# Kernel optimization log

Hardware: AMD Instinct MI355X
Metric: run time of the kernel (lower is better)

Reference implementation:

```python
import jax, jax.numpy as jnp
import numpy as np


def _construct_adj(adj, weight_cross_time):
    # adj: (N, N); weight_cross_time: (S-1, N, N) -> local_adj: (S*N, S*N)
    N = adj.shape[0]
    S = weight_cross_time.shape[0] + 1
    local_adj = jnp.zeros((S * N, S * N), dtype=adj.dtype)
    for i in range(S):  # diagonal blocks (small fixed loop over strides)
        local_adj = local_adj.at[i * N:(i + 1) * N, i * N:(i + 1) * N].set(adj)
    for k in range(S - 1):  # cross-time blocks, symmetric placement
        wk = weight_cross_time[k]
        local_adj = local_adj.at[k * N:(k + 1) * N, (k + 1) * N:(k + 2) * N].set(wk)
        local_adj = local_adj.at[(k + 1) * N:(k + 2) * N, k * N:(k + 1) * N].set(wk.T)
    return local_adj


def setup_inputs() -> dict:
    key = jax.random.key(0)
    k1, k2, k3, k4 = jax.random.split(key, 4)
    N, S, B, Cin, Cout = 1024, 3, 32, 64, 64
    # xavier_uniform-like scales for the learned adjacency parameters
    s_adj = float(np.sqrt(6.0 / (N + N)))
    x = jax.random.normal(k1, (S * N, B, Cin), dtype=jnp.float32)
    adj = jax.random.uniform(k2, (N, N), dtype=jnp.float32, minval=-s_adj, maxval=s_adj)
    weight_cross_time = jax.random.uniform(k3, (S - 1, N, N), dtype=jnp.float32, minval=-s_adj, maxval=s_adj)
    s_fc = float(np.sqrt(1.0 / Cin))
    W = jax.random.uniform(k4, (Cin, 2 * Cout), dtype=jnp.float32, minval=-s_fc, maxval=s_fc)
    b = jnp.zeros((2 * Cout,), dtype=jnp.float32)
    return {"x": x, "adj": adj, "weight_cross_time": weight_cross_time, "W": W, "b": b}


def reference(x, adj, weight_cross_time, W, b):
    # Faithful translation of gcn_operation.forward with activation='GLU'.
    Cout = W.shape[-1] // 2
    local_adj = _construct_adj(adj, weight_cross_time)          # (S*N, S*N)
    h = jnp.einsum('nm,mbc->nbc', local_adj, x)                  # (S*N, B, Cin)
    lhs_rhs = h @ W + b                                          # (S*N, B, 2*Cout)
    lhs, rhs = lhs_rhs[..., :Cout], lhs_rhs[..., Cout:]
    return lhs * jax.nn.sigmoid(rhs)                             # (S*N, B, Cout)
```

## Files before the change

kernel.cpp:

```cpp
#include <hip/hip_runtime.h>

typedef unsigned short u16;
typedef unsigned int   u32;
typedef __attribute__((ext_vector_type(8))) short short8;
typedef __attribute__((ext_vector_type(4))) float f32x4;

__device__ __forceinline__ u16 f2bf(float f) {
    u32 u = __float_as_uint(f);
    u = (u + 0x7fffu + ((u >> 16) & 1u)) >> 16;
    return (u16)u;
}

__device__ __forceinline__ void gld_lds16(const void* g, void* l) {
    __builtin_amdgcn_global_load_lds(
        (const __attribute__((address_space(1))) u32*)g,
        (__attribute__((address_space(3))) u32*)l, 16, 0, 0);
}

__global__ __launch_bounds__(256) void prep_kernel(
    const float* __restrict__ x, const float* __restrict__ adj,
    const float* __restrict__ wct, const float* __restrict__ W,
    u16* __restrict__ Ab, u16* __restrict__ W0T, u16* __restrict__ W1T,
    u16* __restrict__ Xt, u16* __restrict__ Wt)
{
    __shared__ float tile[64][65];
    const int t = threadIdx.x;
    const int bid = blockIdx.x;

    if (bid < 3072) {
        const int i4 = bid * 256 + t;
        const float4 v = (i4 < 262144) ? ((const float4*)adj)[i4]
                                       : ((const float4*)wct)[i4 - 262144];
        ushort4 o;
        o.x = f2bf(v.x); o.y = f2bf(v.y); o.z = f2bf(v.z); o.w = f2bf(v.w);
        ((ushort4*)Ab)[i4] = o;
        return;
    }

    const float* src; u16* dst; int C, R, r0, c0;
    if (bid < 3328)      { const int q = bid - 3072; src = wct;           dst = W0T; C = 1024; R = 1024; r0 = (q & 15) << 6; c0 = (q >> 4) << 6; }
    else if (bid < 3584) { const int q = bid - 3328; src = wct + 1048576; dst = W1T; C = 1024; R = 1024; r0 = (q & 15) << 6; c0 = (q >> 4) << 6; }
    else if (bid < 5120) { const int q = bid - 3584; src = x;             dst = Xt;  C = 2048; R = 3072; r0 = (q % 48) << 6; c0 = (q / 48) << 6; }
    else                 { const int q = bid - 5120; src = W;             dst = Wt;  C = 128;  R = 64;   r0 = 0;             c0 = q << 6; }

#pragma unroll
    for (int it = 0; it < 4; ++it) {
        const int f4 = it * 256 + t;
        const int r  = f4 >> 4;
        const int c4 = (f4 & 15) << 2;
        const float4 v = *(const float4*)&src[(size_t)(r0 + r) * C + c0 + c4];
        tile[r][c4]     = v.x; tile[r][c4 + 1] = v.y;
        tile[r][c4 + 2] = v.z; tile[r][c4 + 3] = v.w;
    }
    __syncthreads();
#pragma unroll
    for (int it = 0; it < 4; ++it) {
        const int f4 = it * 256 + t;
        const int u  = f4 >> 4;
        const int v4 = (f4 & 15) << 2;
        ushort4 o;
        o.x = f2bf(tile[v4][u]);     o.y = f2bf(tile[v4 + 1][u]);
        o.z = f2bf(tile[v4 + 2][u]); o.w = f2bf(tile[v4 + 3][u]);
        *(ushort4*)&dst[(size_t)(c0 + u) * R + r0 + v4] = o;
    }
}

__global__ __launch_bounds__(256, 3) void gemm_h_kernel(
    const u16* __restrict__ Ab,  const u16* __restrict__ W0b,
    const u16* __restrict__ W1b, const u16* __restrict__ W0T,
    const u16* __restrict__ W1T, const u16* __restrict__ Xt,
    const u16* __restrict__ Wt,  const float* __restrict__ bias,
    float* __restrict__ out)
{
    __shared__ u16 Asm[64 * 64];
    __shared__ u16 Bsm[128 * 64];
    __shared__ u16 Wsm[128 * 64];
    __shared__ float Bias_sm[128];

    const int tid = threadIdx.x;
    const int bid = blockIdx.x;
    const int xcd = bid & 7;
    const int idx = bid >> 3;
    const int i   = idx >> 5;
    const int idp = idx & 31;
    const int row0 = (idp & 15) << 6;
    const int nt   = xcd * 2 + (idp >> 4);
    const int col0 = nt << 7;

    const int l    = tid & 63;
    const int w    = tid >> 6;
    const int wr   = ((tid >> 7) & 1) << 5;
    const int wc   = ((tid >> 6) & 1) << 6;
    const int lrow = l & 15;
    const int g16  = l >> 4;
    const int rsw  = lrow & 7;

    {
        u16* wdst = Wsm + ((tid & ~63) << 3);
#pragma unroll
        for (int p = 0; p < 4; ++p) {
            const int flat = p * 256 + tid;
            const int row = flat >> 3, slot = flat & 7;
            gld_lds16(Wt + row * 64 + ((slot ^ (row & 7)) << 3), wdst + p * 2048);
        }
        if (tid < 128) Bias_sm[tid] = bias[tid];
    }

    const int sub  = tid >> 3;
    const int srck = ((tid & 7) ^ (sub & 7)) << 3;
    u16* AsmW = Asm + ((tid >> 6) << 9);
    u16* BsmW = Bsm + ((tid >> 6) << 9);

    f32x4 acc[2][4] = {};

    auto run_term = [&](const u16* __restrict__ Amat, const u16* __restrict__ Bmat) {
        for (int k0 = 0; k0 < 1024; k0 += 64) {
            const u16* ga = Amat + (size_t)sub * 1024 + k0 + srck;
            gld_lds16(ga,             AsmW);
            gld_lds16(ga + 32 * 1024, AsmW + 2048);
            const u16* gb = Bmat + (size_t)sub * 3072 + k0 + srck;
            gld_lds16(gb,             BsmW);
            gld_lds16(gb + 32 * 3072, BsmW + 2048);
            gld_lds16(gb + 64 * 3072, BsmW + 4096);
            gld_lds16(gb + 96 * 3072, BsmW + 6144);
            __syncthreads();

            short8 af[2][2], bfr[2][4];
#pragma unroll
            for (int kk = 0; kk < 2; ++kk) {
                const int so = (((kk << 2) | g16) ^ rsw) << 3;
#pragma unroll
                for (int fm = 0; fm < 2; ++fm)
                    af[kk][fm] = *(const short8*)&Asm[(wr + fm * 16 + lrow) * 64 + so];
#pragma unroll
                for (int fn = 0; fn < 4; ++fn)
                    bfr[kk][fn] = *(const short8*)&Bsm[(wc + fn * 16 + lrow) * 64 + so];
            }
#pragma unroll
            for (int kk = 0; kk < 2; ++kk)
#pragma unroll
                for (int fm = 0; fm < 2; ++fm)
#pragma unroll
                    for (int fn = 0; fn < 4; ++fn)
                        acc[fm][fn] = __builtin_amdgcn_mfma_f32_16x16x32_bf16(
                            af[kk][fm], bfr[kk][fn], acc[fm][fn], 0, 0, 0);
            __syncthreads();
        }
    };

    const size_t xbase = (size_t)col0 * 3072;
    if (i == 0) {
        run_term(Ab  + row0 * 1024, Xt + xbase);
        run_term(W0b + row0 * 1024, Xt + xbase + 1024);
    } else if (i == 1) {
        run_term(W0T + row0 * 1024, Xt + xbase);
        run_term(Ab  + row0 * 1024, Xt + xbase + 1024);
        run_term(W1b + row0 * 1024, Xt + xbase + 2048);
    } else {
        run_term(W1T + row0 * 1024, Xt + xbase + 1024);
        run_term(Ab  + row0 * 1024, Xt + xbase + 2048);
    }

    u16* Hsm = Bsm;
#pragma unroll
    for (int fm = 0; fm < 2; ++fm)
#pragma unroll
        for (int fn = 0; fn < 4; ++fn)
#pragma unroll
            for (int r = 0; r < 4; ++r) {
                const int n   = wr + fm * 16 + (g16 << 2) + r;
                const int col = wc + fn * 16 + lrow;
                const int sl2 = ((col >> 3) ^ (n & 7));
                Hsm[n * 128 + (sl2 << 3) + (col & 7)] = f2bf(acc[fm][fn][r]);
            }
    __syncthreads();

    f32x4 acc2[2][8];
#pragma unroll
    for (int fm2 = 0; fm2 < 2; ++fm2)
#pragma unroll
        for (int fn = 0; fn < 8; ++fn) {
            const float bv = Bias_sm[fn * 16 + lrow];
            acc2[fm2][fn] = (f32x4){bv, bv, bv, bv};
        }
#pragma unroll
    for (int kk = 0; kk < 2; ++kk) {
        const int gg = (kk << 2) | g16;
        short8 ah[2], bw[8];
#pragma unroll
        for (int fm2 = 0; fm2 < 2; ++fm2) {
            const int rowp = (w << 5) + (fm2 << 4) + lrow;
            const int b = rowp >> 6, n = rowp & 63;
            const int sl2 = ((b << 3) | gg) ^ (n & 7);
            ah[fm2] = *(const short8*)&Hsm[n * 128 + (sl2 << 3)];
        }
#pragma unroll
        for (int fn = 0; fn < 8; ++fn) {
            const int c = (fn << 4) + lrow;
            const int sl2 = gg ^ (c & 7);
            bw[fn] = *(const short8*)&Wsm[c * 64 + (sl2 << 3)];
        }
#pragma unroll
        for (int fm2 = 0; fm2 < 2; ++fm2)
#pragma unroll
            for (int fn = 0; fn < 8; ++fn)
                acc2[fm2][fn] = __builtin_amdgcn_mfma_f32_16x16x32_bf16(
                    ah[fm2], bw[fn], acc2[fm2][fn], 0, 0, 0);
    }

    const int n0g = i * 1024 + row0;
    const int b0  = nt << 1;
#pragma unroll
    for (int fm2 = 0; fm2 < 2; ++fm2)
#pragma unroll
        for (int fn = 0; fn < 4; ++fn)
#pragma unroll
            for (int r = 0; r < 4; ++r) {
                const int rowp = (w << 5) + (fm2 << 4) + (g16 << 2) + r;
                const int b = rowp >> 6, nl = rowp & 63;
                const float lhs = acc2[fm2][fn][r];
                const float rhs = acc2[fm2][fn + 4][r];
                const float sg  = 1.0f / (1.0f + __expf(-rhs));
                const int c = (fn << 4) + lrow;
                out[((size_t)(n0g + nl) * 32 + (b0 + b)) * 64 + c] = lhs * sg;
            }
}

extern "C" void kernel_launch(void* const* d_in, const int* in_sizes, int n_in,
                              void* d_out, int out_size, void* d_ws, size_t ws_size,
                              hipStream_t stream)
{
    const float* x    = (const float*)d_in[0];
    const float* adj  = (const float*)d_in[1];
    const float* wct  = (const float*)d_in[2];
    const float* W    = (const float*)d_in[3];
    const float* bias = (const float*)d_in[4];
    float* out = (float*)d_out;

    char* ws = (char*)d_ws;
    u16* Xt  = (u16*)ws;
    u16* Ab  = (u16*)(ws + 12582912);
    u16* W0b = Ab + 1048576;
    u16* W1b = Ab + 2097152;
    u16* W0T = (u16*)(ws + 18874368);
    u16* W1T = W0T + 1048576;
    u16* Wt  = (u16*)(ws + 23068672);

    prep_kernel<<<5122, 256, 0, stream>>>(x, adj, wct, W, Ab, W0T, W1T, Xt, Wt);
    gemm_h_kernel<<<768, 256, 0, stream>>>(Ab, W0b, W1b, W0T, W1T, Xt, Wt, bias, out);
}
```

Baseline: 59.91 us.

## Double-buffer LDS tiles in GEMM main loop and defer W staging to epilogue

The GEMM k-loop now uses ping-pong LDS buffers for the A and B tiles. The next tile's global-to-LDS loads are issued before the MFMAs on the current tile, which drops one barrier per iteration and lets memory latency overlap compute, including across term boundaries. The W tile is no longer kept in its own LDS array for the whole kernel; it is loaded into the freed A buffer after the main loop. Total LDS per block grows (48KB+ vs 40KB), which may limit occupancy at 3 blocks/CU, and the W load now sits on the critical path before the second GEMM.

Measured after the change: 57.63 us. 1.04x faster.

```diff
diff --git a/kernel.cpp b/kernel.cpp
--- a/kernel.cpp
+++ b/kernel.cpp
@@ -72,9 +72,8 @@
     const u16* __restrict__ Wt,  const float* __restrict__ bias,
     float* __restrict__ out)
 {
-    __shared__ u16 Asm[64 * 64];
-    __shared__ u16 Bsm[128 * 64];
-    __shared__ u16 Wsm[128 * 64];
+    __shared__ u16 Adb[8192];
+    __shared__ u16 Bdb[16384];
     __shared__ float Bias_sm[128];
 
     const int tid = threadIdx.x;
@@ -95,73 +94,87 @@
     const int g16  = l >> 4;
     const int rsw  = lrow & 7;
 
-    {
-        u16* wdst = Wsm + ((tid & ~63) << 3);
-#pragma unroll
-        for (int p = 0; p < 4; ++p) {
-            const int flat = p * 256 + tid;
-            const int row = flat >> 3, slot = flat & 7;
-            gld_lds16(Wt + row * 64 + ((slot ^ (row & 7)) << 3), wdst + p * 2048);
-        }
-        if (tid < 128) Bias_sm[tid] = bias[tid];
-    }
-
     const int sub  = tid >> 3;
     const int srck = ((tid & 7) ^ (sub & 7)) << 3;
-    u16* AsmW = Asm + ((tid >> 6) << 9);
-    u16* BsmW = Bsm + ((tid >> 6) << 9);
-
+    const int wofs = w << 9;
+
+    if (tid < 128) Bias_sm[tid] = bias[tid];
+
+    u16 *Ac = Adb, *Ap = Adb + 4096, *Bc = Bdb, *Bp = Bdb + 8192;
     f32x4 acc[2][4] = {};
 
-    auto run_term = [&](const u16* __restrict__ Amat, const u16* __restrict__ Bmat) {
-        for (int k0 = 0; k0 < 1024; k0 += 64) {
-            const u16* ga = Amat + (size_t)sub * 1024 + k0 + srck;
-            gld_lds16(ga,             AsmW);
-            gld_lds16(ga + 32 * 1024, AsmW + 2048);
-            const u16* gb = Bmat + (size_t)sub * 3072 + k0 + srck;
-            gld_lds16(gb,             BsmW);
-            gld_lds16(gb + 32 * 3072, BsmW + 2048);
-            gld_lds16(gb + 64 * 3072, BsmW + 4096);
-            gld_lds16(gb + 96 * 3072, BsmW + 6144);
-            __syncthreads();
-
-            short8 af[2][2], bfr[2][4];
-#pragma unroll
-            for (int kk = 0; kk < 2; ++kk) {
-                const int so = (((kk << 2) | g16) ^ rsw) << 3;
-#pragma unroll
-                for (int fm = 0; fm < 2; ++fm)
-                    af[kk][fm] = *(const short8*)&Asm[(wr + fm * 16 + lrow) * 64 + so];
+    auto stageA = [&](u16* dst, const u16* ta, int kel) {
+        const u16* ga = ta + (size_t)sub * 1024 + kel + srck;
+        gld_lds16(ga,             dst + wofs);
+        gld_lds16(ga + 32 * 1024, dst + wofs + 2048);
+    };
+    auto stageB = [&](u16* dst, const u16* tb, int kel) {
+        const u16* gb = tb + (size_t)sub * 3072 + kel + srck;
+        gld_lds16(gb,             dst + wofs);
+        gld_lds16(gb + 32 * 3072, dst + wofs + 2048);
+        gld_lds16(gb + 64 * 3072, dst + wofs + 4096);
+        gld_lds16(gb + 96 * 3072, dst + wofs + 6144);
+    };
+    auto step = [&](const u16* pfa, const u16* pfb, int kel, int do_pf) {
+        if (do_pf) { stageA(Ap, pfa, kel); stageB(Bp, pfb, kel); }
+        short8 af[2][2], bfr[2][4];
+#pragma unroll
+        for (int kk = 0; kk < 2; ++kk) {
+            const int so = (((kk << 2) | g16) ^ rsw) << 3;
+#pragma unroll
+            for (int fm = 0; fm < 2; ++fm)
+                af[kk][fm] = *(const short8*)&Ac[(wr + fm * 16 + lrow) * 64 + so];
+#pragma unroll
+            for (int fn = 0; fn < 4; ++fn)
+                bfr[kk][fn] = *(const short8*)&Bc[(wc + fn * 16 + lrow) * 64 + so];
+        }
+#pragma unroll
+        for (int kk = 0; kk < 2; ++kk)
+#pragma unroll
+            for (int fm = 0; fm < 2; ++fm)
 #pragma unroll
                 for (int fn = 0; fn < 4; ++fn)
-                    bfr[kk][fn] = *(const short8*)&Bsm[(wc + fn * 16 + lrow) * 64 + so];
-            }
-#pragma unroll
-            for (int kk = 0; kk < 2; ++kk)
-#pragma unroll
-                for (int fm = 0; fm < 2; ++fm)
-#pragma unroll
-                    for (int fn = 0; fn < 4; ++fn)
-                        acc[fm][fn] = __builtin_amdgcn_mfma_f32_16x16x32_bf16(
-                            af[kk][fm], bfr[kk][fn], acc[fm][fn], 0, 0, 0);
-            __syncthreads();
-        }
+                    acc[fm][fn] = __builtin_amdgcn_mfma_f32_16x16x32_bf16(
+                        af[kk][fm], bfr[kk][fn], acc[fm][fn], 0, 0, 0);
+        __syncthreads();
+        u16* t;
+        t = Ac; Ac = Ap; Ap = t;
+        t = Bc; Bc = Bp; Bp = t;
+    };
+    auto run16 = [&](const u16* ta, const u16* tb,
+                     const u16* na, const u16* nb, int hn) {
+        for (int k = 1; k < 16; ++k) step(ta, tb, k << 6, 1);
+        step(na, nb, 0, hn);
     };
 
     const size_t xbase = (size_t)col0 * 3072;
+    const u16 *a0, *b0, *a1, *b1, *a2 = 0, *b2 = 0;
+    int three = 0;
     if (i == 0) {
-        run_term(Ab  + row0 * 1024, Xt + xbase);
-        run_term(W0b + row0 * 1024, Xt + xbase + 1024);
+        a0 = Ab  + row0 * 1024; b0 = Xt + xbase;
+        a1 = W0b + row0 * 1024; b1 = Xt + xbase + 1024;
     } else if (i == 1) {
-        run_term(W0T + row0 * 1024, Xt + xbase);
-        run_term(Ab  + row0 * 1024, Xt + xbase + 1024);
-        run_term(W1b + row0 * 1024, Xt + xbase + 2048);
+        a0 = W0T + row0 * 1024; b0 = Xt + xbase;
+        a1 = Ab  + row0 * 1024; b1 = Xt + xbase + 1024;
+        a2 = W1b + row0 * 1024; b2 = Xt + xbase + 2048;
+        three = 1;
     } else {
-        run_term(W1T + row0 * 1024, Xt + xbase + 1024);
-        run_term(Ab  + row0 * 1024, Xt + xbase + 2048);
-    }
-
-    u16* Hsm = Bsm;
+        a0 = W1T + row0 * 1024; b0 = Xt + xbase + 1024;
+        a1 = Ab  + row0 * 1024; b1 = Xt + xbase + 2048;
+    }
+
+    stageA(Ac, a0, 0); stageB(Bc, b0, 0);
+    __syncthreads();
+    run16(a0, b0, a1, b1, 1);
+    if (three) { run16(a1, b1, a2, b2, 1); run16(a2, b2, 0, 0, 0); }
+    else       { run16(a1, b1, 0, 0, 0); }
+
+    u16* Wsm = Adb;
+    u16* Hsm = Bdb;
+#pragma unroll
+    for (int p = 0; p < 4; ++p)
+        gld_lds16(Wt + (size_t)(p * 32 + sub) * 64 + srck,
+                  Adb + p * 2048 + wofs);
 #pragma unroll
     for (int fm = 0; fm < 2; ++fm)
 #pragma unroll
@@ -209,7 +222,7 @@
     }
 
     const int n0g = i * 1024 + row0;
-    const int b0  = nt << 1;
+    const int b0i = nt << 1;
 #pragma unroll
     for (int fm2 = 0; fm2 < 2; ++fm2)
 #pragma unroll
@@ -222,7 +235,7 @@
                 const float rhs = acc2[fm2][fn + 4][r];
                 const float sg  = 1.0f / (1.0f + __expf(-rhs));
                 const int c = (fn << 4) + lrow;
-                out[((size_t)(n0g + nl) * 32 + (b0 + b)) * 64 + c] = lhs * sg;
+                out[((size_t)(n0g + nl) * 32 + (b0i + b)) * 64 + c] = lhs * sg;
             }
 }
 
```

## Retile adjacency into MFMA fragment order, load A to registers, double-buffer B

Applied to the files above, without the earlier changes.

Prep now writes the adjacency and the transposed cross-time weights in a fragment-tiled layout, so the GEMM kernel can load A operands straight into registers with coalesced 16-byte loads and skip LDS for them. The GEMM tile changes from 64 rows by 128 columns to 128 rows by one batch (64 columns). B tiles are double-buffered in LDS, with a software prefetch that crosses term boundaries and explicit vmcnt waits in place of the full syncthreads pair. This aims to overlap global loads with MFMA and cut LDS traffic. The costs are more register pressure from holding the prefetched A fragments and hand-tuned waitcnt logic that could be fragile.

New measurement: 63.27 us. 5.6% more time.

```diff
diff --git a/kernel.cpp b/kernel.cpp
--- a/kernel.cpp
+++ b/kernel.cpp
@@ -15,6 +15,10 @@
     __builtin_amdgcn_global_load_lds(
         (const __attribute__((address_space(1))) u32*)g,
         (__attribute__((address_space(3))) u32*)l, 16, 0, 0);
+}
+
+__device__ __forceinline__ int ridx(int r, int k) {
+    return ((((r >> 4) << 7) + (k >> 3)) << 7) + ((r & 15) << 3) + (k & 7);
 }
 
 __global__ __launch_bounds__(256) void prep_kernel(
@@ -33,15 +37,19 @@
                                        : ((const float4*)wct)[i4 - 262144];
         ushort4 o;
         o.x = f2bf(v.x); o.y = f2bf(v.y); o.z = f2bf(v.z); o.w = f2bf(v.w);
-        ((ushort4*)Ab)[i4] = o;
+        const int m  = i4 >> 18;
+        const int lf = i4 & 262143;
+        const int r  = lf >> 8;
+        const int k  = (lf & 255) << 2;
+        *(ushort4*)&Ab[m * 1048576 + ridx(r, k)] = o;
         return;
     }
 
-    const float* src; u16* dst; int C, R, r0, c0;
-    if (bid < 3328)      { const int q = bid - 3072; src = wct;           dst = W0T; C = 1024; R = 1024; r0 = (q & 15) << 6; c0 = (q >> 4) << 6; }
-    else if (bid < 3584) { const int q = bid - 3328; src = wct + 1048576; dst = W1T; C = 1024; R = 1024; r0 = (q & 15) << 6; c0 = (q >> 4) << 6; }
-    else if (bid < 5120) { const int q = bid - 3584; src = x;             dst = Xt;  C = 2048; R = 3072; r0 = (q % 48) << 6; c0 = (q / 48) << 6; }
-    else                 { const int q = bid - 5120; src = W;             dst = Wt;  C = 128;  R = 64;   r0 = 0;             c0 = q << 6; }
+    const float* src; u16* dst; int C, R, r0, c0, retile;
+    if (bid < 3328)      { const int q = bid - 3072; src = wct;           dst = W0T; C = 1024; R = 1024; r0 = (q & 15) << 6; c0 = (q >> 4) << 6; retile = 1; }
+    else if (bid < 3584) { const int q = bid - 3328; src = wct + 1048576; dst = W1T; C = 1024; R = 1024; r0 = (q & 15) << 6; c0 = (q >> 4) << 6; retile = 1; }
+    else if (bid < 5120) { const int q = bid - 3584; src = x;             dst = Xt;  C = 2048; R = 3072; r0 = (q % 48) << 6; c0 = (q / 48) << 6; retile = 0; }
+    else                 { const int q = bid - 5120; src = W;             dst = Wt;  C = 128;  R = 64;   r0 = 0;             c0 = q << 6;        retile = 0; }
 
 #pragma unroll
     for (int it = 0; it < 4; ++it) {
@@ -61,7 +69,8 @@
         ushort4 o;
         o.x = f2bf(tile[v4][u]);     o.y = f2bf(tile[v4 + 1][u]);
         o.z = f2bf(tile[v4 + 2][u]); o.w = f2bf(tile[v4 + 3][u]);
-        *(ushort4*)&dst[(size_t)(c0 + u) * R + r0 + v4] = o;
+        if (retile) *(ushort4*)&dst[ridx(c0 + u, r0 + v4)] = o;
+        else        *(ushort4*)&dst[(size_t)(c0 + u) * R + r0 + v4] = o;
     }
 }
 
@@ -72,9 +81,8 @@
     const u16* __restrict__ Wt,  const float* __restrict__ bias,
     float* __restrict__ out)
 {
-    __shared__ u16 Asm[64 * 64];
-    __shared__ u16 Bsm[128 * 64];
-    __shared__ u16 Wsm[128 * 64];
+    __shared__ u16 Bdb[8192];
+    __shared__ u16 Wsm[8192];
     __shared__ float Bias_sm[128];
 
     const int tid = threadIdx.x;
@@ -83,20 +91,16 @@
     const int idx = bid >> 3;
     const int i   = idx >> 5;
     const int idp = idx & 31;
-    const int row0 = (idp & 15) << 6;
-    const int nt   = xcd * 2 + (idp >> 4);
-    const int col0 = nt << 7;
+    const int nt   = (xcd << 2) + (idp & 3);
+    const int row0 = (idp >> 2) << 7;
 
     const int l    = tid & 63;
     const int w    = tid >> 6;
-    const int wr   = ((tid >> 7) & 1) << 5;
-    const int wc   = ((tid >> 6) & 1) << 6;
     const int lrow = l & 15;
     const int g16  = l >> 4;
-    const int rsw  = lrow & 7;
 
     {
-        u16* wdst = Wsm + ((tid & ~63) << 3);
+        u16* wdst = Wsm + (w << 9);
 #pragma unroll
         for (int p = 0; p < 4; ++p) {
             const int flat = p * 256 + tid;
@@ -106,35 +110,76 @@
         if (tid < 128) Bias_sm[tid] = bias[tid];
     }
 
-    const int sub  = tid >> 3;
-    const int srck = ((tid & 7) ^ (sub & 7)) << 3;
-    u16* AsmW = Asm + ((tid >> 6) << 9);
-    u16* BsmW = Bsm + ((tid >> 6) << 9);
+    const int brow = tid >> 3;
+    const int srck = ((tid & 7) ^ (brow & 7)) << 3;
+    auto stageB = [&](u16* buf, const u16* tb, int k0) {
+        const u16* g0 = tb + (size_t)brow * 3072 + k0 + srck;
+        gld_lds16(g0,             buf + (w << 9));
+        gld_lds16(g0 + 32 * 3072, buf + (w << 9) + 2048);
+    };
+
+    const int rbw = w << 1;
+    auto loadA4 = [&](short8* d, const u16* ta, int k0) {
+        const u16* base = ta + (((rbw << 7) + (k0 >> 3)) << 7) + (l << 3);
+        d[0] = *(const short8*)(base);
+        d[1] = *(const short8*)(base + 512);
+        d[2] = *(const short8*)(base + 16384);
+        d[3] = *(const short8*)(base + 16384 + 512);
+    };
 
     f32x4 acc[2][4] = {};
-
-    auto run_term = [&](const u16* __restrict__ Amat, const u16* __restrict__ Bmat) {
-        for (int k0 = 0; k0 < 1024; k0 += 64) {
-            const u16* ga = Amat + (size_t)sub * 1024 + k0 + srck;
-            gld_lds16(ga,             AsmW);
-            gld_lds16(ga + 32 * 1024, AsmW + 2048);
-            const u16* gb = Bmat + (size_t)sub * 3072 + k0 + srck;
-            gld_lds16(gb,             BsmW);
-            gld_lds16(gb + 32 * 3072, BsmW + 2048);
-            gld_lds16(gb + 64 * 3072, BsmW + 4096);
-            gld_lds16(gb + 96 * 3072, BsmW + 6144);
-            __syncthreads();
-
-            short8 af[2][2], bfr[2][4];
+    short8 aC[4], aN[4];
+
+    const size_t xbase = (size_t)nt * 64 * 3072;
+    const u16 *ca, *cb, *na, *nb, *fa = nullptr, *fb = nullptr;
+    int nterms;
+    if (i == 0) {
+        ca = Ab  + (row0 << 10); cb = Xt + xbase;
+        na = W0b + (row0 << 10); nb = Xt + xbase + 1024;
+        nterms = 2;
+    } else if (i == 1) {
+        ca = W0T + (row0 << 10); cb = Xt + xbase;
+        na = Ab  + (row0 << 10); nb = Xt + xbase + 1024;
+        fa = W1b + (row0 << 10); fb = Xt + xbase + 2048;
+        nterms = 3;
+    } else {
+        ca = W1T + (row0 << 10); cb = Xt + xbase + 1024;
+        na = Ab  + (row0 << 10); nb = Xt + xbase + 2048;
+        nterms = 2;
+    }
+
+    stageB(Bdb, cb, 0);
+    loadA4(aC, ca, 0);
+
+    for (int t = 0; t < nterms; ++t) {
+#pragma unroll
+        for (int k = 0; k < 16; ++k) {
+            u16* bufc = Bdb + ((k & 1) << 12);
+            u16* bufp = Bdb + (((k + 1) & 1) << 12);
+            const u16* pa = (k < 15) ? ca : na;
+            const u16* pb = (k < 15) ? cb : nb;
+            const int pk0 = (k < 15) ? ((k + 1) << 6) : 0;
+            const bool pf = (k < 15) || (na != nullptr);
+
+            __builtin_amdgcn_s_barrier();
+            if (pf) {
+                stageB(bufp, pb, pk0);
+                loadA4(aN, pa, pk0);
+                asm volatile("s_waitcnt vmcnt(10)" ::: "memory");
+            } else {
+                asm volatile("s_waitcnt vmcnt(4)" ::: "memory");
+            }
+            __builtin_amdgcn_s_barrier();
+
+            short8 bfr[2][4];
 #pragma unroll
             for (int kk = 0; kk < 2; ++kk) {
-                const int so = (((kk << 2) | g16) ^ rsw) << 3;
-#pragma unroll
-                for (int fm = 0; fm < 2; ++fm)
-                    af[kk][fm] = *(const short8*)&Asm[(wr + fm * 16 + lrow) * 64 + so];
-#pragma unroll
-                for (int fn = 0; fn < 4; ++fn)
-                    bfr[kk][fn] = *(const short8*)&Bsm[(wc + fn * 16 + lrow) * 64 + so];
+                const int kidx = (kk << 2) | g16;
+#pragma unroll
+                for (int fn = 0; fn < 4; ++fn) {
+                    const int col = (fn << 4) + lrow;
+                    bfr[kk][fn] = *(const short8*)&bufc[(col << 6) + ((kidx ^ (col & 7)) << 3)];
+                }
             }
 #pragma unroll
             for (int kk = 0; kk < 2; ++kk)
@@ -143,44 +188,32 @@
 #pragma unroll
                     for (int fn = 0; fn < 4; ++fn)
                         acc[fm][fn] = __builtin_amdgcn_mfma_f32_16x16x32_bf16(
-                            af[kk][fm], bfr[kk][fn], acc[fm][fn], 0, 0, 0);
-            __syncthreads();
-        }
-    };
-
-    const size_t xbase = (size_t)col0 * 3072;
-    if (i == 0) {
-        run_term(Ab  + row0 * 1024, Xt + xbase);
-        run_term(W0b + row0 * 1024, Xt + xbase + 1024);
-    } else if (i == 1) {
-        run_term(W0T + row0 * 1024, Xt + xbase);
-        run_term(Ab  + row0 * 1024, Xt + xbase + 1024);
-        run_term(W1b + row0 * 1024, Xt + xbase + 2048);
-    } else {
-        run_term(W1T + row0 * 1024, Xt + xbase + 1024);
-        run_term(Ab  + row0 * 1024, Xt + xbase + 2048);
-    }
-
-    u16* Hsm = Bsm;
+                            aC[(fm << 1) | kk], bfr[kk][fn], acc[fm][fn], 0, 0, 0);
+#pragma unroll
+            for (int j = 0; j < 4; ++j) aC[j] = aN[j];
+        }
+        ca = na; cb = nb; na = fa; nb = fb; fa = nullptr; fb = nullptr;
+    }
+
+    __syncthreads();
+    u16* Hsm = Bdb;
 #pragma unroll
     for (int fm = 0; fm < 2; ++fm)
 #pragma unroll
         for (int fn = 0; fn < 4; ++fn)
 #pragma unroll
             for (int r = 0; r < 4; ++r) {
-                const int n   = wr + fm * 16 + (g16 << 2) + r;
-                const int col = wc + fn * 16 + lrow;
-                const int sl2 = ((col >> 3) ^ (n & 7));
-                Hsm[n * 128 + (sl2 << 3) + (col & 7)] = f2bf(acc[fm][fn][r]);
-            }
-    __syncthreads();
+                const int n   = (w << 5) + (fm << 4) + (g16 << 2) + r;
+                const int cin = (fn << 4) + lrow;
+                Hsm[(n << 6) + (((cin >> 3) ^ (n & 7)) << 3) + (cin & 7)] = f2bf(acc[fm][fn][r]);
+            }
 
     f32x4 acc2[2][8];
 #pragma unroll
     for (int fm2 = 0; fm2 < 2; ++fm2)
 #pragma unroll
         for (int fn = 0; fn < 8; ++fn) {
-            const float bv = Bias_sm[fn * 16 + lrow];
+            const float bv = Bias_sm[(fn << 4) + lrow];
             acc2[fm2][fn] = (f32x4){bv, bv, bv, bv};
         }
 #pragma unroll
@@ -189,16 +222,13 @@
         short8 ah[2], bw[8];
 #pragma unroll
         for (int fm2 = 0; fm2 < 2; ++fm2) {
-            const int rowp = (w << 5) + (fm2 << 4) + lrow;
-            const int b = rowp >> 6, n = rowp & 63;
-            const int sl2 = ((b << 3) | gg) ^ (n & 7);
-            ah[fm2] = *(const short8*)&Hsm[n * 128 + (sl2 << 3)];
+            const int n = (w << 5) + (fm2 << 4) + lrow;
+            ah[fm2] = *(const short8*)&Hsm[(n << 6) + ((gg ^ (n & 7)) << 3)];
         }
 #pragma unroll
         for (int fn = 0; fn < 8; ++fn) {
             const int c = (fn << 4) + lrow;
-            const int sl2 = gg ^ (c & 7);
-            bw[fn] = *(const short8*)&Wsm[c * 64 + (sl2 << 3)];
+            bw[fn] = *(const short8*)&Wsm[(c << 6) + ((gg ^ (c & 7)) << 3)];
         }
 #pragma unroll
         for (int fm2 = 0; fm2 < 2; ++fm2)
@@ -208,21 +238,19 @@
                     ah[fm2], bw[fn], acc2[fm2][fn], 0, 0, 0);
     }
 
-    const int n0g = i * 1024 + row0;
-    const int b0  = nt << 1;
+    const int n0g = (i << 10) + row0;
 #pragma unroll
     for (int fm2 = 0; fm2 < 2; ++fm2)
 #pragma unroll
         for (int fn = 0; fn < 4; ++fn)
 #pragma unroll
             for (int r = 0; r < 4; ++r) {
-                const int rowp = (w << 5) + (fm2 << 4) + (g16 << 2) + r;
-                const int b = rowp >> 6, nl = rowp & 63;
+                const int nl = (w << 5) + (fm2 << 4) + (g16 << 2) + r;
                 const float lhs = acc2[fm2][fn][r];
                 const float rhs = acc2[fm2][fn + 4][r];
                 const float sg  = 1.0f / (1.0f + __expf(-rhs));
                 const int c = (fn << 4) + lrow;
-                out[((size_t)(n0g + nl) * 32 + (b0 + b)) * 64 + c] = lhs * sg;
+                out[((size_t)(n0g + nl) * 32 + nt) * 64 + c] = lhs * sg;
             }
 }
 
```

## Double-buffer GEMM with 128x128 tiles and 32x32x16 MFMA

Applied to the files above, without the earlier changes.

Rewrites the main GEMM kernel to use 128x128 output tiles, shared-memory double buffering with async global-to-LDS prefetch and explicit vmcnt waits, and 32x32x16 bf16 MFMA instead of 16x16x32. The grid drops from 768 to 384 blocks, and the 3-term row segment is scheduled first. The aim is to hide load latency, raise arithmetic intensity and cut barrier overhead. The cost is higher LDS and register use, which lowers occupancy to 2 blocks per CU, and fewer blocks than the roughly 256 CUs may leave the second wave partially idle.

After: 70.92 us. 18.4% more time.

```diff
diff --git a/kernel.cpp b/kernel.cpp
--- a/kernel.cpp
+++ b/kernel.cpp
@@ -3,7 +3,7 @@
 typedef unsigned short u16;
 typedef unsigned int   u32;
 typedef __attribute__((ext_vector_type(8))) short short8;
-typedef __attribute__((ext_vector_type(4))) float f32x4;
+typedef __attribute__((ext_vector_type(16))) float f32x16;
 
 __device__ __forceinline__ u16 f2bf(float f) {
     u32 u = __float_as_uint(f);
@@ -65,164 +65,189 @@
     }
 }
 
-__global__ __launch_bounds__(256, 3) void gemm_h_kernel(
+__global__ __launch_bounds__(256, 2) void gemm_h_kernel(
     const u16* __restrict__ Ab,  const u16* __restrict__ W0b,
     const u16* __restrict__ W1b, const u16* __restrict__ W0T,
     const u16* __restrict__ W1T, const u16* __restrict__ Xt,
     const u16* __restrict__ Wt,  const float* __restrict__ bias,
     float* __restrict__ out)
 {
-    __shared__ u16 Asm[64 * 64];
-    __shared__ u16 Bsm[128 * 64];
-    __shared__ u16 Wsm[128 * 64];
-    __shared__ float Bias_sm[128];
+    __shared__ u16 Adb[16384];
+    __shared__ u16 Bdb[16384];
 
     const int tid = threadIdx.x;
     const int bid = blockIdx.x;
     const int xcd = bid & 7;
     const int idx = bid >> 3;
-    const int i   = idx >> 5;
-    const int idp = idx & 31;
-    const int row0 = (idp & 15) << 6;
-    const int nt   = xcd * 2 + (idp >> 4);
-    const int col0 = nt << 7;
+    const int seg = idx >> 4;
+    const int i   = (seg == 0) ? 1 : ((seg == 1) ? 0 : 2);
+    const int sub16 = idx & 15;
+    const int mt_l  = sub16 >> 1;
+    const int nt    = (xcd << 1) + (sub16 & 1);
+    const int row0  = mt_l << 7;
+    const int col0  = nt << 7;
 
     const int l    = tid & 63;
     const int w    = tid >> 6;
-    const int wr   = ((tid >> 7) & 1) << 5;
-    const int wc   = ((tid >> 6) & 1) << 6;
-    const int lrow = l & 15;
-    const int g16  = l >> 4;
-    const int rsw  = lrow & 7;
+    const int wr   = ((w >> 1) & 1) << 6;
+    const int wc   = (w & 1) << 6;
+    const int l31  = l & 31;
+    const int lh   = l >> 5;
+    const int l7   = l31 & 7;
+
+    const int srow = tid >> 3;
+    const int sswz = ((tid & 7) ^ (srow & 7)) << 3;
+    auto stage = [&](u16* Abuf, u16* Bbuf, const u16* ta, const u16* tb, int k0) {
+#pragma unroll
+        for (int p = 0; p < 4; ++p) {
+            const int row = (p << 5) + srow;
+            gld_lds16(ta + (size_t)row * 1024 + k0 + sswz,
+                      Abuf + (p << 12) + ((tid >> 6) << 9) + 0);
+            gld_lds16(tb + (size_t)row * 3072 + k0 + sswz,
+                      Bbuf + (p << 12) + ((tid >> 6) << 9) + 0);
+        }
+    };
+
+    auto stage2 = [&](u16* Abuf, u16* Bbuf, const u16* ta, const u16* tb, int k0) {
+#pragma unroll
+        for (int p = 0; p < 4; ++p) {
+            const int row = (p << 5) + srow;
+            u16* db = Abuf + (p << 11) + ((tid & 192) << 3);
+            u16* eb = Bbuf + (p << 11) + ((tid & 192) << 3);
+            gld_lds16(ta + (size_t)row * 1024 + k0 + sswz, db);
+            gld_lds16(tb + (size_t)row * 3072 + k0 + sswz, eb);
+        }
+    };
+
+    f32x16 acc00 = {}, acc01 = {}, acc10 = {}, acc11 = {};
+
+    const size_t rofs = (size_t)row0 * 1024;
+    const size_t xb   = (size_t)col0 * 3072;
+    const u16 *ca, *cb, *na, *nb, *fa = nullptr, *fb = nullptr;
+    int nterms;
+    if (i == 0) {
+        ca = Ab  + rofs; cb = Xt + xb;
+        na = W0b + rofs; nb = Xt + xb + 1024;
+        nterms = 2;
+    } else if (i == 1) {
+        ca = W0T + rofs; cb = Xt + xb;
+        na = Ab  + rofs; nb = Xt + xb + 1024;
+        fa = W1b + rofs; fb = Xt + xb + 2048;
+        nterms = 3;
+    } else {
+        ca = W1T + rofs; cb = Xt + xb + 1024;
+        na = Ab  + rofs; nb = Xt + xb + 2048;
+        nterms = 2;
+    }
+
+    u16 *Ac = Adb, *Ap = Adb + 8192, *Bc = Bdb, *Bp = Bdb + 8192;
+
+    auto step = [&](const u16* pfa, const u16* pfb, int pk0, bool pf) {
+        __builtin_amdgcn_s_barrier();
+        if (pf) {
+            stage2(Ap, Bp, pfa, pfb, pk0);
+            asm volatile("s_waitcnt vmcnt(8)" ::: "memory");
+        } else {
+            asm volatile("s_waitcnt vmcnt(0)" ::: "memory");
+        }
+        __builtin_amdgcn_s_barrier();
+
+        __builtin_amdgcn_s_setprio(1);
+#pragma unroll
+        for (int ks = 0; ks < 4; ++ks) {
+            const int off = (((ks << 1) | lh) ^ l7) << 3;
+            const short8 a0 = *(const short8*)&Ac[((wr + l31) << 6) + off];
+            const short8 a1 = *(const short8*)&Ac[((wr + 32 + l31) << 6) + off];
+            const short8 b0 = *(const short8*)&Bc[((wc + l31) << 6) + off];
+            const short8 b1 = *(const short8*)&Bc[((wc + 32 + l31) << 6) + off];
+            acc00 = __builtin_amdgcn_mfma_f32_32x32x16_bf16(a0, b0, acc00, 0, 0, 0);
+            acc01 = __builtin_amdgcn_mfma_f32_32x32x16_bf16(a0, b1, acc01, 0, 0, 0);
+            acc10 = __builtin_amdgcn_mfma_f32_32x32x16_bf16(a1, b0, acc10, 0, 0, 0);
+            acc11 = __builtin_amdgcn_mfma_f32_32x32x16_bf16(a1, b1, acc11, 0, 0, 0);
+        }
+        __builtin_amdgcn_s_setprio(0);
+        u16* t;
+        t = Ac; Ac = Ap; Ap = t;
+        t = Bc; Bc = Bp; Bp = t;
+    };
+
+    stage2(Ac, Bc, ca, cb, 0);
+    for (int t = 0; t < nterms; ++t) {
+        for (int k = 0; k < 15; ++k) step(ca, cb, (k + 1) << 6, true);
+        step(na, nb, 0, na != nullptr);
+        ca = na; cb = nb; na = fa; nb = fb; fa = nullptr; fb = nullptr;
+    }
+
+    __syncthreads();
+    u16* Wsm = Adb;
+    u16* Hsm = Bdb;
+#pragma unroll
+    for (int p = 0; p < 4; ++p) {
+        const int row = (p << 5) + srow;
+        gld_lds16(Wt + (size_t)row * 64 + sswz,
+                  Adb + (p << 11) + ((tid & 192) << 3));
+    }
 
     {
-        u16* wdst = Wsm + ((tid & ~63) << 3);
-#pragma unroll
-        for (int p = 0; p < 4; ++p) {
-            const int flat = p * 256 + tid;
-            const int row = flat >> 3, slot = flat & 7;
-            gld_lds16(Wt + row * 64 + ((slot ^ (row & 7)) << 3), wdst + p * 2048);
-        }
-        if (tid < 128) Bias_sm[tid] = bias[tid];
-    }
-
-    const int sub  = tid >> 3;
-    const int srck = ((tid & 7) ^ (sub & 7)) << 3;
-    u16* AsmW = Asm + ((tid >> 6) << 9);
-    u16* BsmW = Bsm + ((tid >> 6) << 9);
-
-    f32x4 acc[2][4] = {};
-
-    auto run_term = [&](const u16* __restrict__ Amat, const u16* __restrict__ Bmat) {
-        for (int k0 = 0; k0 < 1024; k0 += 64) {
-            const u16* ga = Amat + (size_t)sub * 1024 + k0 + srck;
-            gld_lds16(ga,             AsmW);
-            gld_lds16(ga + 32 * 1024, AsmW + 2048);
-            const u16* gb = Bmat + (size_t)sub * 3072 + k0 + srck;
-            gld_lds16(gb,             BsmW);
-            gld_lds16(gb + 32 * 3072, BsmW + 2048);
-            gld_lds16(gb + 64 * 3072, BsmW + 4096);
-            gld_lds16(gb + 96 * 3072, BsmW + 6144);
-            __syncthreads();
-
-            short8 af[2][2], bfr[2][4];
-#pragma unroll
-            for (int kk = 0; kk < 2; ++kk) {
-                const int so = (((kk << 2) | g16) ^ rsw) << 3;
-#pragma unroll
-                for (int fm = 0; fm < 2; ++fm)
-                    af[kk][fm] = *(const short8*)&Asm[(wr + fm * 16 + lrow) * 64 + so];
-#pragma unroll
-                for (int fn = 0; fn < 4; ++fn)
-                    bfr[kk][fn] = *(const short8*)&Bsm[(wc + fn * 16 + lrow) * 64 + so];
-            }
-#pragma unroll
-            for (int kk = 0; kk < 2; ++kk)
-#pragma unroll
-                for (int fm = 0; fm < 2; ++fm)
-#pragma unroll
-                    for (int fn = 0; fn < 4; ++fn)
-                        acc[fm][fn] = __builtin_amdgcn_mfma_f32_16x16x32_bf16(
-                            af[kk][fm], bfr[kk][fn], acc[fm][fn], 0, 0, 0);
-            __syncthreads();
-        }
-    };
-
-    const size_t xbase = (size_t)col0 * 3072;
-    if (i == 0) {
-        run_term(Ab  + row0 * 1024, Xt + xbase);
-        run_term(W0b + row0 * 1024, Xt + xbase + 1024);
-    } else if (i == 1) {
-        run_term(W0T + row0 * 1024, Xt + xbase);
-        run_term(Ab  + row0 * 1024, Xt + xbase + 1024);
-        run_term(W1b + row0 * 1024, Xt + xbase + 2048);
-    } else {
-        run_term(W1T + row0 * 1024, Xt + xbase + 1024);
-        run_term(Ab  + row0 * 1024, Xt + xbase + 2048);
-    }
-
-    u16* Hsm = Bsm;
-#pragma unroll
-    for (int fm = 0; fm < 2; ++fm)
-#pragma unroll
-        for (int fn = 0; fn < 4; ++fn)
-#pragma unroll
-            for (int r = 0; r < 4; ++r) {
-                const int n   = wr + fm * 16 + (g16 << 2) + r;
-                const int col = wc + fn * 16 + lrow;
-                const int sl2 = ((col >> 3) ^ (n & 7));
-                Hsm[n * 128 + (sl2 << 3) + (col & 7)] = f2bf(acc[fm][fn][r]);
-            }
+        const f32x16 aa[2][2] = {{acc00, acc01}, {acc10, acc11}};
+#pragma unroll
+        for (int fm = 0; fm < 2; ++fm)
+#pragma unroll
+            for (int fn = 0; fn < 2; ++fn)
+#pragma unroll
+                for (int r = 0; r < 16; ++r) {
+                    const int n   = wr + (fm << 5) + (r & 3) + ((r >> 2) << 3) + (lh << 2);
+                    const int col = wc + (fn << 5) + l31;
+                    const int b   = col >> 6, cin = col & 63;
+                    const int rp  = (b << 7) + n;
+                    Hsm[(rp << 6) + ((((cin >> 3) ^ (rp & 7))) << 3) + (cin & 7)] =
+                        f2bf(aa[fm][fn][r]);
+                }
+    }
     __syncthreads();
 
-    f32x4 acc2[2][8];
+    const float bc0 = bias[l31], bc1 = bias[l31 + 32],
+                bc2 = bias[l31 + 64], bc3 = bias[l31 + 96];
+    f32x16 q00, q01, q02, q03, q10, q11, q12, q13;
+#pragma unroll
+    for (int r = 0; r < 16; ++r) {
+        q00[r] = bc0; q01[r] = bc1; q02[r] = bc2; q03[r] = bc3;
+        q10[r] = bc0; q11[r] = bc1; q12[r] = bc2; q13[r] = bc3;
+    }
+#pragma unroll
+    for (int ks = 0; ks < 4; ++ks) {
+        const int off = (((ks << 1) | lh) ^ l7) << 3;
+        const short8 ah0 = *(const short8*)&Hsm[(((w << 6) + l31) << 6) + off];
+        const short8 ah1 = *(const short8*)&Hsm[(((w << 6) + 32 + l31) << 6) + off];
+        const short8 bw0 = *(const short8*)&Wsm[((l31) << 6) + off];
+        const short8 bw1 = *(const short8*)&Wsm[((32 + l31) << 6) + off];
+        const short8 bw2 = *(const short8*)&Wsm[((64 + l31) << 6) + off];
+        const short8 bw3 = *(const short8*)&Wsm[((96 + l31) << 6) + off];
+        q00 = __builtin_amdgcn_mfma_f32_32x32x16_bf16(ah0, bw0, q00, 0, 0, 0);
+        q01 = __builtin_amdgcn_mfma_f32_32x32x16_bf16(ah0, bw1, q01, 0, 0, 0);
+        q02 = __builtin_amdgcn_mfma_f32_32x32x16_bf16(ah0, bw2, q02, 0, 0, 0);
+        q03 = __builtin_amdgcn_mfma_f32_32x32x16_bf16(ah0, bw3, q03, 0, 0, 0);
+        q10 = __builtin_amdgcn_mfma_f32_32x32x16_bf16(ah1, bw0, q10, 0, 0, 0);
+        q11 = __builtin_amdgcn_mfma_f32_32x32x16_bf16(ah1, bw1, q11, 0, 0, 0);
+        q12 = __builtin_amdgcn_mfma_f32_32x32x16_bf16(ah1, bw2, q12, 0, 0, 0);
+        q13 = __builtin_amdgcn_mfma_f32_32x32x16_bf16(ah1, bw3, q13, 0, 0, 0);
+    }
+
+    const int n0g = (i << 10) + row0;
+    const int b0i = nt << 1;
+    const f32x16 qa[2][4] = {{q00, q01, q02, q03}, {q10, q11, q12, q13}};
 #pragma unroll
     for (int fm2 = 0; fm2 < 2; ++fm2)
 #pragma unroll
-        for (int fn = 0; fn < 8; ++fn) {
-            const float bv = Bias_sm[fn * 16 + lrow];
-            acc2[fm2][fn] = (f32x4){bv, bv, bv, bv};
-        }
-#pragma unroll
-    for (int kk = 0; kk < 2; ++kk) {
-        const int gg = (kk << 2) | g16;
-        short8 ah[2], bw[8];
-#pragma unroll
-        for (int fm2 = 0; fm2 < 2; ++fm2) {
-            const int rowp = (w << 5) + (fm2 << 4) + lrow;
-            const int b = rowp >> 6, n = rowp & 63;
-            const int sl2 = ((b << 3) | gg) ^ (n & 7);
-            ah[fm2] = *(const short8*)&Hsm[n * 128 + (sl2 << 3)];
-        }
-#pragma unroll
-        for (int fn = 0; fn < 8; ++fn) {
-            const int c = (fn << 4) + lrow;
-            const int sl2 = gg ^ (c & 7);
-            bw[fn] = *(const short8*)&Wsm[c * 64 + (sl2 << 3)];
-        }
-#pragma unroll
-        for (int fm2 = 0; fm2 < 2; ++fm2)
-#pragma unroll
-            for (int fn = 0; fn < 8; ++fn)
-                acc2[fm2][fn] = __builtin_amdgcn_mfma_f32_16x16x32_bf16(
-                    ah[fm2], bw[fn], acc2[fm2][fn], 0, 0, 0);
-    }
-
-    const int n0g = i * 1024 + row0;
-    const int b0  = nt << 1;
-#pragma unroll
-    for (int fm2 = 0; fm2 < 2; ++fm2)
-#pragma unroll
-        for (int fn = 0; fn < 4; ++fn)
-#pragma unroll
-            for (int r = 0; r < 4; ++r) {
-                const int rowp = (w << 5) + (fm2 << 4) + (g16 << 2) + r;
-                const int b = rowp >> 6, nl = rowp & 63;
-                const float lhs = acc2[fm2][fn][r];
-                const float rhs = acc2[fm2][fn + 4][r];
+        for (int fn2 = 0; fn2 < 2; ++fn2)
+#pragma unroll
+            for (int r = 0; r < 16; ++r) {
+                const int rowp = (w << 6) + (fm2 << 5) + (r & 3) + ((r >> 2) << 3) + (lh << 2);
+                const int b = rowp >> 7, nl = rowp & 127;
+                const float lhs = qa[fm2][fn2][r];
+                const float rhs = qa[fm2][fn2 + 2][r];
                 const float sg  = 1.0f / (1.0f + __expf(-rhs));
-                const int c = (fn << 4) + lrow;
-                out[((size_t)(n0g + nl) * 32 + (b0 + b)) * 64 + c] = lhs * sg;
+                out[((size_t)(n0g + nl) * 32 + b0i + b) * 64 + (fn2 << 5) + l31] = lhs * sg;
             }
 }
 
@@ -247,5 +272,5 @@
     u16* Wt  = (u16*)(ws + 23068672);
 
     prep_kernel<<<5122, 256, 0, stream>>>(x, adj, wct, W, Ab, W0T, W1T, Xt, Wt);
-    gemm_h_kernel<<<768, 256, 0, stream>>>(Ab, W0b, W1b, W0T, W1T, Xt, Wt, bias, out);
-}
+    gemm_h_kernel<<<384, 256, 0, stream>>>(Ab, W0b, W1b, W0T, W1T, Xt, Wt, bias, out);
+}
```
